# Kernel tuning notes

Hardware: AMD Instinct MI355X
Metric: run time of the kernel (lower is better)

## Reference

```python
import jax, jax.numpy as jnp
import numpy as np

B, T, K, H = 8, 1024, 128, 8
TOP_K = 64
KS = 5  # conv kernel size for Q/K
DN = ('NCH', 'OIH', 'NCH')


def setup_inputs() -> dict:
    key = jax.random.key(0)
    ks = jax.random.split(key, 9)
    s = 0.05
    return {
        'x': jax.random.normal(ks[0], (B, T, K), jnp.float32),
        'Wq': jax.random.normal(ks[1], (K * H, K, KS), jnp.float32) * s,
        'bq': jax.random.normal(ks[2], (K * H,), jnp.float32) * s,
        'Wk': jax.random.normal(ks[3], (K * H, K, KS), jnp.float32) * s,
        'bk': jax.random.normal(ks[4], (K * H,), jnp.float32) * s,
        'Wv': jax.random.normal(ks[5], (K * H, K, 1), jnp.float32) * s,
        'bv': jax.random.normal(ks[6], (K * H,), jnp.float32) * s,
        'Wu': jax.random.normal(ks[7], (K, K * H), jnp.float32) * s,
        'bu': jax.random.normal(ks[8], (K,), jnp.float32) * s,
    }


def _prep(z, b, k, h, t, scale):
    # z: (b, k*h, t) conv output; torch view(b,k,h,t) then transposes -> (b,h,t,k)
    z = z.reshape(b, k, h, t)
    z = jnp.transpose(z, (0, 2, 3, 1)) * scale  # (b, h, t, k)
    # torch: transpose(1,2).contiguous().view(b*h, t, k) -- replicate exactly
    z = jnp.transpose(z, (0, 2, 1, 3)).reshape(b * h, t, k)
    return z


def reference(x, Wq, bq, Wk, bk, Wv, bv, Wu, bu):
    b, t, k = x.shape
    h = H
    xc = jnp.transpose(x, (0, 2, 1))  # (b, k, t)
    # causal left-pad KS-1 for Q/K convs; V is pointwise (kernel 1)
    q = jax.lax.conv_general_dilated(xc, Wq, (1,), [(KS - 1, 0)], dimension_numbers=DN) + bq[None, :, None]
    kk = jax.lax.conv_general_dilated(xc, Wk, (1,), [(KS - 1, 0)], dimension_numbers=DN) + bk[None, :, None]
    v = jax.lax.conv_general_dilated(xc, Wv, (1,), [(0, 0)], dimension_numbers=DN) + bv[None, :, None]
    scale = k ** -0.25
    q = _prep(q, b, k, h, t, scale)
    kk = _prep(kk, b, k, h, t, scale)
    v = _prep(v, b, k, h, t, 1.0)
    w = jnp.einsum('btk,bsk->bts', q, kk)  # (b*h, t, t)
    # top-k sparsification: keep entries >= k-th largest per row, else row min
    largest, _ = jax.lax.top_k(w, TOP_K)
    thresh = jnp.min(largest, axis=-1, keepdims=True)
    row_min = jnp.min(w, axis=-1, keepdims=True)
    w = jnp.where(w >= thresh, w, row_min)
    # causal mask (strict upper triangle -> -inf)
    causal = jnp.triu(jnp.ones((t, t), bool), 1)
    w = jnp.where(causal[None], -jnp.inf, w)
    w = jax.nn.softmax(w, axis=-1)
    out = jnp.einsum('bts,bsk->btk', w, v)  # (b*h, t, k)
    out = out.reshape(b, h, t, k)
    out = jnp.transpose(out, (0, 2, 1, 3)).reshape(b, t, k * h)
    return out @ Wu.T + bu
```

## Files before the change

### kernel.cpp

```cpp
#include <hip/hip_runtime.h>
#include <hip/hip_fp16.h>
#include <cstdint>

using f16 = _Float16;
typedef __attribute__((ext_vector_type(8))) _Float16 f16x8;
typedef __attribute__((ext_vector_type(4))) _Float16 f16x4;
typedef __attribute__((ext_vector_type(4))) float f32x4;

#define MFMA16(a, b, c) __builtin_amdgcn_mfma_f32_16x16x32_f16((a), (b), (c), 0, 0, 0)

__device__ __forceinline__ f16x8 ldfrag(const f16* p) { return *(const f16x8*)p; }

__device__ __forceinline__ void dma16(const f16* g, f16* l) {
  __builtin_amdgcn_global_load_lds(
      (const __attribute__((address_space(1))) void*)g,
      (__attribute__((address_space(3))) void*)l, 16, 0, 0);
}
__device__ __forceinline__ void wait_vm0() {
  asm volatile("s_waitcnt vmcnt(0)" ::: "memory");
}
__device__ __forceinline__ void wait_lgkm0() {
  asm volatile("s_waitcnt lgkmcnt(0)" ::: "memory");
}
__device__ __forceinline__ void wait_vm4() {
  asm volatile("s_waitcnt vmcnt(4)" ::: "memory");
}
__device__ __forceinline__ void wait_vm2() {
  asm volatile("s_waitcnt vmcnt(2)" ::: "memory");
}

static const int64_t NX = 1048576;
static const int64_t NW = 655360;
static const int64_t NV = 131072;

__global__ __launch_bounds__(256) void k0_prep(
    const float* __restrict__ x, const float* __restrict__ Wq,
    const float* __restrict__ Wk, const float* __restrict__ Wv,
    const float* __restrict__ Wu,
    f16* __restrict__ xh, f16* __restrict__ xl,
    f16* __restrict__ Wqh, f16* __restrict__ Wql,
    f16* __restrict__ Wkh, f16* __restrict__ Wkl,
    f16* __restrict__ Wvb, f16* __restrict__ Wub) {
  int64_t i = (int64_t)blockIdx.x * 256 + threadIdx.x;
  if (i < NX) {
    const float v = x[i];
    const f16 h = (f16)v;
    xh[i] = h; xl[i] = (f16)(v - (float)h);
  } else if (i < NX + NW) {
    int64_t d = i - NX;
    int j = (int)(d >> 17);
    int rem = (int)(d & 131071);
    int o = rem >> 7, c = rem & 127;
    const float v = Wq[(int64_t)(o * 128 + c) * 5 + j];
    const f16 h = (f16)v;
    Wqh[d] = h; Wql[d] = (f16)(v - (float)h);
  } else if (i < NX + 2 * NW) {
    int64_t d = i - NX - NW;
    int j = (int)(d >> 17);
    int rem = (int)(d & 131071);
    int o = rem >> 7, c = rem & 127;
    const float v = Wk[(int64_t)(o * 128 + c) * 5 + j];
    const f16 h = (f16)v;
    Wkh[d] = h; Wkl[d] = (f16)(v - (float)h);
  } else if (i < NX + 2 * NW + NV) {
    int64_t d = i - NX - 2 * NW;
    Wvb[d] = (f16)Wv[d];
  } else {
    int64_t d = i - NX - 2 * NW - NV;
    Wub[d] = (f16)Wu[d];
  }
}

#define STAGE_QK(DST, PASS, VALEXPR)                                    \
  {                                                                     \
    __syncthreads();                                                    \
    _Pragma("unroll")                                                   \
    for (int nt = 0; nt < 8; ++nt) {                                    \
      const int o = o0 + nt * 16 + lo;                                  \
      const int kcl = (o >> 3) & 63, hh = o & 7;                        \
      _Pragma("unroll")                                                 \
      for (int rtl = 0; rtl < 2; ++rtl) {                               \
        const int rt = (PASS) * 2 + rtl;                                \
        _Pragma("unroll")                                               \
        for (int r = 0; r < 4; ++r) {                                   \
          const int t2l = (rtl * 16 + quad * 4 + r) * 8 + hh;           \
          lds[t2l * 72 + kcl] = (VALEXPR);                              \
        }                                                               \
      }                                                                 \
    }                                                                   \
    __syncthreads();                                                    \
    _Pragma("unroll")                                                   \
    for (int p = 0; p < 8; ++p) {                                       \
      const int idx = p * 256 + tid;                                    \
      const int a = idx >> 3, c8 = (idx & 7) * 8;                       \
      *(f16x8*)(DST + ((int64_t)m * 1024 + t2b + (PASS) * 256 + a) * 128 + \
                half * 64 + c8) = *(const f16x8*)&lds[a * 72 + c8];     \
    }                                                                   \
  }

__global__ __launch_bounds__(256) void k1_conv(
    const f16* __restrict__ xh, const f16* __restrict__ xl,
    const f16* __restrict__ Wqh, const f16* __restrict__ Wql,
    const f16* __restrict__ Wkh, const f16* __restrict__ Wkl,
    const f16* __restrict__ Wvb,
    const float* __restrict__ bq, const float* __restrict__ bk,
    const float* __restrict__ bv,
    f16* __restrict__ q3h, f16* __restrict__ q3l,
    f16* __restrict__ k3h, f16* __restrict__ k3l,
    f16* __restrict__ v3T) {
  __shared__ f16 shm[36384];
  f16* const wbuf = shm;
  f16* const xbuf = shm + 18432;
  f16* const lds  = shm;
  const int tid = threadIdx.x;
  const int w = tid >> 6, lane = tid & 63;
  const int quad = lane >> 4, lo = lane & 15;
  const int r0 = blockIdx.x * 64;
  const int bb = r0 >> 10;
  const int m  = r0 >> 7;
  const int t2b = (r0 & 127) * 8;
  const int tloc = r0 & 1023;
  const int half = blockIdx.y;
  const int isK = blockIdx.z;
  const int o0 = half * 512 + w * 128;

  const f16* Wh = isK ? Wkh : Wqh;
  const f16* Wl = isK ? Wkl : Wql;
  const float* bias = isK ? bk : bq;

#pragma unroll
  for (int p = 0; p < 9; ++p) {
    const int u = p * 256 + tid;
    if (u < 2176) {
      const int row = u >> 5, tz = (u >> 4) & 1, c8 = (u & 15) * 8;
      int lt = tloc - 4 + row;
      if (lt < 0) lt = 0;
      const f16* src = (tz ? xl : xh) + ((int64_t)(bb * 1024 + lt)) * 128 + c8;
      *(f16x8*)&xbuf[row * 264 + tz * 128 + c8] = *(const f16x8*)src;
    }
  }
  __syncthreads();

  const int64_t wlane = (int64_t)(lane & 15) * 128 + (lane >> 4) * 8;

  if (!isK) {
    f32x4 av[4][8];
#pragma unroll
    for (int rt = 0; rt < 4; ++rt)
#pragma unroll
      for (int i = 0; i < 8; ++i)
#pragma unroll
        for (int r = 0; r < 4; ++r) av[rt][i][r] = 0.f;

#pragma unroll
    for (int g = 0; g < 4; ++g) {
#pragma unroll
      for (int s = 0; s < 2; ++s) {
        const int64_t vsrc = (int64_t)(o0 + (g * 2 + s) * 16) * 128 + wlane;
#pragma unroll
        for (int kk = 0; kk < 4; ++kk)
          dma16(Wvb + vsrc + kk * 32, wbuf + w * 4096 + s * 2048 + kk * 512);
      }
      wait_vm0();
#pragma unroll
      for (int kk = 0; kk < 4; ++kk) {
        f16x8 a[4];
#pragma unroll
        for (int rt = 0; rt < 4; ++rt)
          a[rt] = *(const f16x8*)&xbuf[(rt * 16 + lo + 4) * 264 + kk * 32 +
                                       quad * 8];
#pragma unroll
        for (int s = 0; s < 2; ++s) {
          const f16x8 bv8 = *(const f16x8*)&wbuf[w * 4096 + s * 2048 + kk * 512 +
                                                 quad * 128 + lo * 8];
#pragma unroll
          for (int rt = 0; rt < 4; ++rt)
            av[rt][g * 2 + s] = MFMA16(a[rt], bv8, av[rt][g * 2 + s]);
        }
      }
      wait_lgkm0();
    }
    __syncthreads();
#pragma unroll
    for (int pass = 0; pass < 2; ++pass) {
#pragma unroll
      for (int nt = 0; nt < 8; ++nt) {
        const int o = o0 + nt * 16 + lo;
        const float vbv = bv[o];
        const int kcl = (o >> 3) & 63, hh = o & 7;
#pragma unroll
        for (int rtl = 0; rtl < 2; ++rtl)
#pragma unroll
          for (int r = 0; r < 4; ++r) {
            const int t2l = (rtl * 16 + quad * 4 + r) * 8 + hh;
            lds[kcl * 264 + t2l] = (f16)(av[pass * 2 + rtl][nt][r] + vbv);
          }
      }
      __syncthreads();
#pragma unroll
      for (int p = 0; p < 8; ++p) {
        const int idx = p * 256 + tid;
        const int kcl = idx >> 5, t8 = (idx & 31) * 8;
        *(f16x8*)(v3T + ((int64_t)m * 128 + half * 64 + kcl) * 1024 + t2b +
                  pass * 256 + t8) = *(const f16x8*)&lds[kcl * 264 + t8];
      }
      __syncthreads();
    }
  }

  f32x4 aq[4][8];
#pragma unroll
  for (int rt = 0; rt < 4; ++rt)
#pragma unroll
    for (int i = 0; i < 8; ++i)
#pragma unroll
      for (int r = 0; r < 4; ++r) { aq[rt][i][r] = 0.f; }

  for (int j = 0; j < 5; ++j) {
    const bool z0 = (tloc == 0);
#pragma unroll
    for (int nt = 0; nt < 8; ++nt) {
      const int64_t wsrc =
          (int64_t)j * 131072 + (int64_t)(o0 + nt * 16) * 128 + wlane;
#pragma unroll
      for (int kk = 0; kk < 4; ++kk) {
        dma16(Wh + wsrc + kk * 32, wbuf + w * 4096 + kk * 512);
        dma16(Wl + wsrc + kk * 32, wbuf + w * 4096 + 2048 + kk * 512);
      }
      wait_vm4();
#pragma unroll
      for (int kk = 0; kk < 4; ++kk) {
        if (kk == 2) wait_vm0();
        const f16x8 bh =
            *(const f16x8*)&wbuf[w * 4096 + kk * 512 + quad * 128 + lo * 8];
        const f16x8 bl =
            *(const f16x8*)&wbuf[w * 4096 + 2048 + kk * 512 + quad * 128 + lo * 8];
#pragma unroll
        for (int rt = 0; rt < 4; ++rt) {
          f16x8 ah = *(const f16x8*)&xbuf[(rt * 16 + lo + j) * 264 + kk * 32 +
                                          quad * 8];
          f16x8 al = *(const f16x8*)&xbuf[(rt * 16 + lo + j) * 264 + 128 +
                                          kk * 32 + quad * 8];
          if (rt == 0 && z0 && (lo + j < 4)) {
#pragma unroll
            for (int e = 0; e < 8; ++e) { ah[e] = (f16)0; al[e] = (f16)0; }
          }
          aq[rt][nt] = MFMA16(ah, bh, aq[rt][nt]);
          aq[rt][nt] = MFMA16(ah, bl, aq[rt][nt]);
          aq[rt][nt] = MFMA16(al, bh, aq[rt][nt]);
        }
      }
      wait_lgkm0();
    }
  }

  const float SC = 0.29730177875068026f;
#pragma unroll
  for (int nt = 0; nt < 8; ++nt) {
    const int o = o0 + nt * 16 + lo;
    const float vb = bias[o];
#pragma unroll
    for (int rt = 0; rt < 4; ++rt)
#pragma unroll
      for (int r = 0; r < 4; ++r) aq[rt][nt][r] = (aq[rt][nt][r] + vb) * SC;
  }

  if (!isK) {
    STAGE_QK(q3h, 0, (f16)aq[rt][nt][r])
    STAGE_QK(q3h, 1, (f16)aq[rt][nt][r])
    STAGE_QK(q3l, 0, (f16)(aq[rt][nt][r] - (float)(f16)aq[rt][nt][r]))
    STAGE_QK(q3l, 1, (f16)(aq[rt][nt][r] - (float)(f16)aq[rt][nt][r]))
  } else {
    STAGE_QK(k3h, 0, (f16)aq[rt][nt][r])
    STAGE_QK(k3h, 1, (f16)aq[rt][nt][r])
    STAGE_QK(k3l, 0, (f16)(aq[rt][nt][r] - (float)(f16)aq[rt][nt][r]))
    STAGE_QK(k3l, 1, (f16)(aq[rt][nt][r] - (float)(f16)aq[rt][nt][r]))
  }
}

__global__ __launch_bounds__(512, 4) void k234_attn(
    const f16* __restrict__ q3h, const f16* __restrict__ q3l,
    const f16* __restrict__ k3h, const f16* __restrict__ k3l,
    const f16* __restrict__ v3T, f16* __restrict__ A) {
  __shared__ float Sb[16 * 516];
  __shared__ f16 kbuf[16384];
  const int tid = threadIdx.x;
  const int w = tid >> 6, lane = tid & 63;
  const int quad = lane >> 4, lo = lane & 15;
  const int qd = lane & 3, cit = lane >> 2;
  const int qsw = qd ^ ((cit >> 1) & 3);
  const int fro = (lo * 4 + (quad ^ ((lo >> 1) & 3))) * 8;
  const int hid = blockIdx.y * 64 + blockIdx.x;
  const int m = (hid & 7) * 8 + ((hid >> 3) >> 6);
  const int r0 = ((hid >> 3) & 63) * 16;

  const int64_t qoff = ((int64_t)m * 1024 + r0 + lo) * 128;
  f16x8 qh[4], ql[4];
#pragma unroll
  for (int kk = 0; kk < 4; ++kk) {
    qh[kk] = ldfrag(q3h + qoff + kk * 32 + quad * 8);
    ql[kk] = ldfrag(q3l + qoff + kk * 32 + quad * 8);
  }

  unsigned key[2][16];
  unsigned kmn0 = 0xFFFFFFFFu, kmn1 = 0xFFFFFFFFu;

#pragma unroll
  for (int half = 0; half < 2; ++half) {
    f32x4 acc[4];
#pragma unroll
    for (int i = 0; i < 4; ++i)
#pragma unroll
      for (int r = 0; r < 4; ++r) acc[i][r] = 0.f;

    for (int kp = 0; kp < 2; ++kp) {
#pragma unroll
      for (int cc = 0; cc < 4; ++cc) {
        const int c0 = half * 512 + cc * 128;
        const int64_t rowg = (int64_t)(m * 1024 + c0 + w * 16 + cit) * 128;
#pragma unroll
        for (int t = 0; t < 2; ++t) {
          const f16* srcb = t ? k3l : k3h;
#pragma unroll
          for (int kkh = 0; kkh < 2; ++kkh)
            dma16(srcb + rowg + (kp * 2 + kkh) * 32 + qsw * 8,
                  kbuf + (w * 4 + t * 2 + kkh) * 512);
        }
        wait_vm0();
#pragma unroll
        for (int kkh = 0; kkh < 2; ++kkh) {
          const int kkg = kp * 2 + kkh;
          f16x8 bh = *(const f16x8*)(kbuf + (w * 4 + kkh) * 512 + fro);
          f16x8 bl = *(const f16x8*)(kbuf + (w * 4 + 2 + kkh) * 512 + fro);
          acc[cc] = MFMA16(qh[kkg], bh, acc[cc]);
          acc[cc] = MFMA16(qh[kkg], bl, acc[cc]);
          acc[cc] = MFMA16(ql[kkg], bh, acc[cc]);
        }
        wait_lgkm0();
      }
    }
#pragma unroll
    for (int cc = 0; cc < 4; ++cc)
#pragma unroll
      for (int r = 0; r < 4; ++r)
        Sb[(quad * 4 + r) * 516 + cc * 128 + w * 16 + lo] = acc[cc][r];
    __syncthreads();
#pragma unroll
    for (int rr = 0; rr < 2; ++rr) {
      const float4* rp = (const float4*)(Sb + (w * 2 + rr) * 516);
#pragma unroll
      for (int i2 = 0; i2 < 2; ++i2) {
        const float4 f4 = rp[i2 * 64 + lane];
        const float fe[4] = {f4.x, f4.y, f4.z, f4.w};
#pragma unroll
        for (int e = 0; e < 4; ++e) {
          const unsigned u = __builtin_bit_cast(unsigned, fe[e]);
          const unsigned k = (u & 0x80000000u) ? ~u : (u | 0x80000000u);
          key[rr][half * 8 + i2 * 4 + e] = k;
          if (rr == 0) kmn0 = min(kmn0, k); else kmn1 = min(kmn1, k);
        }
      }
    }
    __syncthreads();
  }

  const int64_t vrow = (int64_t)(m * 128 + w * 16 + cit) * 1024;
  const int nkb = (r0 >> 6) + 1;
#define VISSUE(KB, PAIR)                                                 \
  {                                                                      \
    dma16(v3T + vrow + (KB) * 64 + qsw * 8,                              \
          kbuf + (w * 4 + (PAIR) * 2) * 512);                            \
    dma16(v3T + vrow + (KB) * 64 + 32 + qsw * 8,                         \
          kbuf + (w * 4 + (PAIR) * 2 + 1) * 512);                        \
  }
  VISSUE(0, 0)
  if (nkb > 1) VISSUE(1, 1)

  f16* P16 = (f16*)Sb;
  {
#pragma unroll
    for (int off = 32; off; off >>= 1) {
      kmn0 = min(kmn0, (unsigned)__shfl_xor((int)kmn0, off));
      kmn1 = min(kmn1, (unsigned)__shfl_xor((int)kmn1, off));
    }
    unsigned th0 = 0u, th1 = 0u;
    bool d0 = false, d1 = false;
    for (int b = 31; b >= 0; --b) {
      if (!d0) {
        const unsigned c0 = th0 | (1u << b);
        int cnt0 = 0;
#pragma unroll
        for (int i = 0; i < 16; ++i)
          cnt0 += (int)__popcll(__ballot(key[0][i] >= c0));
        if (cnt0 >= 64) { th0 = c0; if (cnt0 == 64) d0 = true; }
      }
      if (!d1) {
        const unsigned c1 = th1 | (1u << b);
        int cnt1 = 0;
#pragma unroll
        for (int i = 0; i < 16; ++i)
          cnt1 += (int)__popcll(__ballot(key[1][i] >= c1));
        if (cnt1 >= 64) { th1 = c1; if (cnt1 == 64) d1 = true; }
      }
      if (d0 && d1) break;
    }

#pragma unroll
    for (int rr = 0; rr < 2; ++rr) {
      const unsigned kth = rr ? th1 : th0;
      const unsigned kmn = rr ? kmn1 : kmn0;
      const int row = w * 2 + rr, t2 = r0 + row;
      const unsigned umn = (kmn & 0x80000000u) ? (kmn ^ 0x80000000u) : ~kmn;
      const float mn = __builtin_bit_cast(float, umn);
      const unsigned ukv = (kth & 0x80000000u) ? (kth ^ 0x80000000u) : ~kth;
      const float kv = __builtin_bit_cast(float, ukv);

      float ev[16];
      float sum = 0.f;
#pragma unroll
      for (int j = 0; j < 16; ++j) {
        const int s = (j >> 3) * 512 + ((j >> 2) & 1) * 256 + lane * 4 + (j & 3);
        const unsigned k = key[rr][j];
        const unsigned uu = (k & 0x80000000u) ? (k ^ 0x80000000u) : ~k;
        const float f = __builtin_bit_cast(float, uu);
        const float ww = (k >= kth) ? f : mn;
        const float x = (s <= t2) ? __expf(ww - kv) : 0.f;
        ev[j] = x;
        sum += x;
      }
      for (int off = 32; off; off >>= 1) sum += __shfl_xor(sum, off);
      const float inv = 1.0f / sum;

      f16* prow = P16 + row * 1032;
#pragma unroll
      for (int hh = 0; hh < 2; ++hh)
#pragma unroll
        for (int i2 = 0; i2 < 2; ++i2) {
          f16x4 pk;
#pragma unroll
          for (int e = 0; e < 4; ++e)
            pk[e] = (f16)(ev[hh * 8 + i2 * 4 + e] * inv);
          *(f16x4*)(prow + hh * 512 + i2 * 256 + lane * 4) = pk;
        }
    }
  }
  __syncthreads();

  {
    f32x4 oa0, oa1;
#pragma unroll
    for (int r = 0; r < 4; ++r) { oa0[r] = 0.f; oa1[r] = 0.f; }
    for (int kb = 0; kb < nkb; ++kb) {
      if (kb + 1 < nkb) wait_vm2();
      else wait_vm0();
      const int pair = kb & 1;
      {
        const f16x8 vf0 = *(const f16x8*)(kbuf + (w * 4 + pair * 2) * 512 + fro);
        const f16x8 vf1 =
            *(const f16x8*)(kbuf + (w * 4 + pair * 2 + 1) * 512 + fro);
        const f16x8 af0 = *(const f16x8*)(P16 + lo * 1032 + kb * 64 + quad * 8);
        const f16x8 af1 =
            *(const f16x8*)(P16 + lo * 1032 + kb * 64 + 32 + quad * 8);
        oa0 = MFMA16(af0, vf0, oa0);
        oa1 = MFMA16(af1, vf1, oa1);
      }
      wait_lgkm0();
      if (kb + 2 < nkb) VISSUE(kb + 2, pair)
    }
#undef VISSUE
#pragma unroll
    for (int r = 0; r < 4; ++r)
      A[((int64_t)m * 1024 + r0 + quad * 4 + r) * 128 + w * 16 + lo] =
          (f16)(oa0[r] + oa1[r]);
  }
}

__global__ __launch_bounds__(256) void k5_proj(
    const f16* __restrict__ A, const f16* __restrict__ Wub,
    const float* __restrict__ bu, float* __restrict__ out) {
  const int w = threadIdx.x >> 6, lane = threadIdx.x & 63;
  const int quad = lane >> 4, lo = lane & 15;
  const int rt = w & 1, ch = w >> 1;
  const int r0 = blockIdx.x * 32 + rt * 16;
  const int r = r0 + lo;
  const int bI = r >> 10, t2 = r & 1023;

  f32x4 acc[4];
#pragma unroll
  for (int i = 0; i < 4; ++i)
#pragma unroll
    for (int rr = 0; rr < 4; ++rr) acc[i][rr] = 0.f;

#pragma unroll 2
  for (int kk = 0; kk < 32; ++kk) {
    const int o = kk * 32 + quad * 8;
    const int j = o >> 7, kc = o & 127;
    f16x8 a = ldfrag(A + (((int64_t)(bI * 8 + j) * 1024 + t2) * 128 + kc));
    f16x8 wb[4];
#pragma unroll
    for (int nt = 0; nt < 4; ++nt)
      wb[nt] = ldfrag(Wub + (int64_t)(ch * 64 + nt * 16 + lo) * 1024 + o);
#pragma unroll
    for (int nt = 0; nt < 4; ++nt) acc[nt] = MFMA16(a, wb[nt], acc[nt]);
  }
#pragma unroll
  for (int nt = 0; nt < 4; ++nt) {
    const int col = ch * 64 + nt * 16 + lo;
    const float bias = bu[col];
#pragma unroll
    for (int rr = 0; rr < 4; ++rr) {
      const int row = r0 + quad * 4 + rr;
      out[(int64_t)row * 128 + col] = acc[nt][rr] + bias;
    }
  }
}

extern "C" void kernel_launch(void* const* d_in, const int* in_sizes, int n_in,
                              void* d_out, int out_size, void* d_ws, size_t ws_size,
                              hipStream_t stream) {
  const float* x  = (const float*)d_in[0];
  const float* Wq = (const float*)d_in[1];
  const float* bq = (const float*)d_in[2];
  const float* Wk = (const float*)d_in[3];
  const float* bk = (const float*)d_in[4];
  const float* Wv = (const float*)d_in[5];
  const float* bv = (const float*)d_in[6];
  const float* Wu = (const float*)d_in[7];
  const float* bu = (const float*)d_in[8];
  float* out = (float*)d_out;

  char* ws = (char*)d_ws;
  f16* xh  = (f16*)ws;  ws += 2097152;
  f16* xl  = (f16*)ws;  ws += 2097152;
  f16* Wqh = (f16*)ws;  ws += 1310720;
  f16* Wql = (f16*)ws;  ws += 1310720;
  f16* Wkh = (f16*)ws;  ws += 1310720;
  f16* Wkl = (f16*)ws;  ws += 1310720;
  f16* Wvb = (f16*)ws;  ws += 262144;
  f16* Wub = (f16*)ws;  ws += 262144;
  f16* q3h = (f16*)ws;  ws += 16777216;
  f16* q3l = (f16*)ws;  ws += 16777216;
  f16* k3h = (f16*)ws;  ws += 16777216;
  f16* k3l = (f16*)ws;  ws += 16777216;
  f16* v3T = (f16*)ws;  ws += 16777216;
  f16* A   = (f16*)ws;  ws += 16777216;

  k0_prep<<<10240, 256, 0, stream>>>(x, Wq, Wk, Wv, Wu,
                                     xh, xl, Wqh, Wql, Wkh, Wkl, Wvb, Wub);

  k1_conv<<<dim3(128, 2, 2), 256, 0, stream>>>(xh, xl, Wqh, Wql, Wkh, Wkl, Wvb,
                                               bq, bk, bv, q3h, q3l, k3h, k3l,
                                               v3T);

  k234_attn<<<dim3(64, 64), 512, 0, stream>>>(q3h, q3l, k3h, k3l, v3T, A);

  k5_proj<<<256, 256, 0, stream>>>(A, Wub, bu, out);

  (void)in_sizes; (void)n_in; (void)out_size; (void)ws_size;
}
```

Baseline: 433.1 us.

## Stream K and V tiles through a 4-slot rolling DMA ring

Replaces the issue-then-wait_vm0 pattern in the QK^T loop with a four-deep rolling ring of per-wave LDS slots. Each 16-byte global-to-LDS load is issued four steps ahead and consumed after a vmcnt(3) wait. The V prefetch continues the same ring, so the first V tiles load during the top-k and softmax phase. This hides global load latency behind MFMA work. In exchange it adds complex index arithmetic and dummy V loads (clamped to block 0) past the end, which are drained at the end.

```diff
diff --git a/kernel.cpp b/kernel.cpp
--- a/kernel.cpp
+++ b/kernel.cpp
@@ -25,8 +25,8 @@
 __device__ __forceinline__ void wait_vm4() {
   asm volatile("s_waitcnt vmcnt(4)" ::: "memory");
 }
-__device__ __forceinline__ void wait_vm2() {
-  asm volatile("s_waitcnt vmcnt(2)" ::: "memory");
+__device__ __forceinline__ void wait_vm3() {
+  asm volatile("s_waitcnt vmcnt(3)" ::: "memory");
 }
 
 static const int64_t NX = 1048576;
@@ -302,6 +302,26 @@
     ql[kk] = ldfrag(q3l + qoff + kk * 32 + quad * 8);
   }
 
+  const int64_t kfb = ((int64_t)m * 1024 + w * 16 + cit) * 128 + qsw * 8;
+  const f16* const khp = k3h + kfb;
+  const f16* const klp = k3l + kfb;
+  f16* const wslot = kbuf + w * 2048;
+  const int64_t vrow = (int64_t)(m * 128 + w * 16 + cit) * 1024 + qsw * 8;
+  const int nkb = (r0 >> 6) + 1;
+  const int NV2 = nkb * 2;
+
+#define KOFF(p)                                                          \
+  ((int64_t)(((p) >> 5) * 512 + (((p) >> 2) & 3) * 128) * 128 +          \
+   ((((p) >> 4) & 1) * 2 + (((p) >> 1) & 1)) * 32)
+#define KISSUE(p)                                                        \
+  dma16(((p)&1 ? klp : khp) + KOFF(p), wslot + ((p)&3) * 512);
+#define VISSUE(v)                                                        \
+  dma16(v3T + vrow + (int64_t)((((v) >> 1) < nkb ? ((v) >> 1) : 0)) * 64 + \
+            ((v)&1) * 32,                                                \
+        wslot + ((v)&3) * 512);
+
+  KISSUE(0) KISSUE(1) KISSUE(2) KISSUE(3)
+
   unsigned key[2][16];
   unsigned kmn0 = 0xFFFFFFFFu, kmn1 = 0xFFFFFFFFu;
 
@@ -313,32 +333,24 @@
 #pragma unroll
       for (int r = 0; r < 4; ++r) acc[i][r] = 0.f;
 
-    for (int kp = 0; kp < 2; ++kp) {
-#pragma unroll
-      for (int cc = 0; cc < 4; ++cc) {
-        const int c0 = half * 512 + cc * 128;
-        const int64_t rowg = (int64_t)(m * 1024 + c0 + w * 16 + cit) * 128;
-#pragma unroll
-        for (int t = 0; t < 2; ++t) {
-          const f16* srcb = t ? k3l : k3h;
-#pragma unroll
-          for (int kkh = 0; kkh < 2; ++kkh)
-            dma16(srcb + rowg + (kp * 2 + kkh) * 32 + qsw * 8,
-                  kbuf + (w * 4 + t * 2 + kkh) * 512);
-        }
-        wait_vm0();
-#pragma unroll
-        for (int kkh = 0; kkh < 2; ++kkh) {
-          const int kkg = kp * 2 + kkh;
-          f16x8 bh = *(const f16x8*)(kbuf + (w * 4 + kkh) * 512 + fro);
-          f16x8 bl = *(const f16x8*)(kbuf + (w * 4 + 2 + kkh) * 512 + fro);
-          acc[cc] = MFMA16(qh[kkg], bh, acc[cc]);
-          acc[cc] = MFMA16(qh[kkg], bl, acc[cc]);
-          acc[cc] = MFMA16(ql[kkg], bh, acc[cc]);
-        }
-        wait_lgkm0();
-      }
-    }
+#pragma unroll
+    for (int ph = 0; ph < 32; ++ph) {
+      const int p = half * 32 + ph;
+      wait_vm3();
+      const f16x8 x = *(const f16x8*)(wslot + (p & 3) * 512 + fro);
+      const int kkg = ((p >> 4) & 1) * 2 + ((p >> 1) & 1);
+      const int cc = (p >> 2) & 3;
+      if ((p & 1) == 0) {
+        acc[cc] = MFMA16(qh[kkg], x, acc[cc]);
+        acc[cc] = MFMA16(ql[kkg], x, acc[cc]);
+      } else {
+        acc[cc] = MFMA16(qh[kkg], x, acc[cc]);
+      }
+      wait_lgkm0();
+      if (p + 4 < 64) { KISSUE(p + 4) }
+      else { VISSUE(p + 4 - 64) }
+    }
+
 #pragma unroll
     for (int cc = 0; cc < 4; ++cc)
 #pragma unroll
@@ -363,18 +375,6 @@
     }
     __syncthreads();
   }
-
-  const int64_t vrow = (int64_t)(m * 128 + w * 16 + cit) * 1024;
-  const int nkb = (r0 >> 6) + 1;
-#define VISSUE(KB, PAIR)                                                 \
-  {                                                                      \
-    dma16(v3T + vrow + (KB) * 64 + qsw * 8,                              \
-          kbuf + (w * 4 + (PAIR) * 2) * 512);                            \
-    dma16(v3T + vrow + (KB) * 64 + 32 + qsw * 8,                         \
-          kbuf + (w * 4 + (PAIR) * 2 + 1) * 512);                        \
-  }
-  VISSUE(0, 0)
-  if (nkb > 1) VISSUE(1, 1)
 
   f16* P16 = (f16*)Sb;
   {
@@ -450,24 +450,19 @@
     f32x4 oa0, oa1;
 #pragma unroll
     for (int r = 0; r < 4; ++r) { oa0[r] = 0.f; oa1[r] = 0.f; }
-    for (int kb = 0; kb < nkb; ++kb) {
-      if (kb + 1 < nkb) wait_vm2();
-      else wait_vm0();
-      const int pair = kb & 1;
-      {
-        const f16x8 vf0 = *(const f16x8*)(kbuf + (w * 4 + pair * 2) * 512 + fro);
-        const f16x8 vf1 =
-            *(const f16x8*)(kbuf + (w * 4 + pair * 2 + 1) * 512 + fro);
-        const f16x8 af0 = *(const f16x8*)(P16 + lo * 1032 + kb * 64 + quad * 8);
-        const f16x8 af1 =
-            *(const f16x8*)(P16 + lo * 1032 + kb * 64 + 32 + quad * 8);
-        oa0 = MFMA16(af0, vf0, oa0);
-        oa1 = MFMA16(af1, vf1, oa1);
-      }
+    for (int v = 0; v < NV2; ++v) {
+      wait_vm3();
+      const f16x8 vf = *(const f16x8*)(wslot + (v & 3) * 512 + fro);
+      const f16x8 af = *(const f16x8*)(P16 + lo * 1032 + v * 32 + quad * 8);
+      if (v & 1) oa1 = MFMA16(af, vf, oa1);
+      else       oa0 = MFMA16(af, vf, oa0);
       wait_lgkm0();
-      if (kb + 2 < nkb) VISSUE(kb + 2, pair)
-    }
+      VISSUE(v + 4)
+    }
+    wait_vm0();
 #undef VISSUE
+#undef KISSUE
+#undef KOFF
 #pragma unroll
     for (int r = 0; r < 4; ++r)
       A[((int64_t)m * 1024 + r0 + quad * 4 + r) * 128 + w * 16 + lo] =
```

Measured after the change: 440.2 us. Within noise of the previous version (+1.6%).
